# Performance work log

Measured on AMD Instinct MI355X. Metric: run time of the kernel, lower is better.

Reference implementation:

```python
import jax, jax.numpy as jnp
import numpy as np

IMG = 448; P = 16; C = 3; D = 512; DC = 8; DS = 4
NH = IMG // P            # 28 patches per side
NPATCH = NH * NH         # 784
PDIM = C * P * P         # 768
BATCH = 32
EPS = 1e-5


def setup_inputs() -> dict:
    key = jax.random.key(0)
    ks = jax.random.split(key, 10)
    def lin(k, fan_in, shape):
        bound = 1.0 / np.sqrt(fan_in)
        return jax.random.uniform(k, shape, jnp.float32, -bound, bound)
    return {
        "images": jax.random.normal(ks[0], (BATCH, C, IMG, IMG), jnp.float32),
        "W_patch": lin(ks[1], PDIM, (PDIM, D)),
        "b_patch": jnp.zeros((D,), jnp.float32),
        "pos_embed": jax.random.normal(ks[2], (1, NPATCH, D), jnp.float32) * 0.02,
        "W_coord": lin(ks[3], D, (D, DC)),
        "b_coord": jnp.zeros((DC,), jnp.float32),
        "W_spinor": lin(ks[4], D, (D, DS)),
        "b_spinor": jnp.zeros((DS,), jnp.float32),
        "W_embed": lin(ks[5], DC, (DC, D)),
        "b_embed": jnp.zeros((D,), jnp.float32),
        "ln_gamma": jnp.ones((D,), jnp.float32),
        "ln_beta": jnp.zeros((D,), jnp.float32),
        "W_out": lin(ks[6], D, (D, D)),
        "b_out": jnp.zeros((D,), jnp.float32),
    }


def reference(images, W_patch, b_patch, pos_embed, W_coord, b_coord,
              W_spinor, b_spinor, W_embed, b_embed,
              ln_gamma, ln_beta, W_out, b_out):
    B = images.shape[0]
    # patchify == F.unfold(kernel=stride=P).transpose(1,2):
    # patches[b, bh*NH+bw, c*P*P + i*P + j] = images[b, c, bh*P+i, bw*P+j]
    patches = images.reshape(B, C, NH, P, NH, P)
    patches = patches.transpose(0, 2, 4, 1, 3, 5).reshape(B, NPATCH, PDIM)
    # patch embed + positional embedding  -> (B, NPATCH, D)
    x = patches @ W_patch + b_patch + pos_embed
    # manifold projection: coords (B,N,DC), spinor (B,N,DS)
    coords = x @ W_coord + b_coord
    spinor = x @ W_spinor + b_spinor
    # K0 scalar bilinear: psi^T psi -> (B, N)
    K0 = jnp.sum(spinor * spinor, axis=-1)
    # embed back from manifold coords -> (B, N, D)
    x_manifold = coords @ W_embed + b_embed
    # K0-modulated remix + residual
    x_enh = x_manifold * K0[..., None] + x
    # output projection: LayerNorm -> Linear
    mu = jnp.mean(x_enh, axis=-1, keepdims=True)
    var = jnp.mean(jnp.square(x_enh - mu), axis=-1, keepdims=True)
    x_norm = (x_enh - mu) * jax.lax.rsqrt(var + EPS) * ln_gamma + ln_beta
    return x_norm @ W_out + b_out
```

## Files before the change

### kernel.cpp

```cpp
#include <hip/hip_runtime.h>
#include <hip/hip_bf16.h>
#include <stdint.h>


typedef __bf16 bf16_t;
typedef bf16_t bf16x8 __attribute__((ext_vector_type(8)));
typedef bf16_t bf16x4 __attribute__((ext_vector_type(4)));
typedef float  f32x4  __attribute__((ext_vector_type(4)));

#define IMG     448
#define PSZ     16
#define NHP     28
#define NPATCH  784
#define PDIM    768
#define DMODEL  512
#define MROWS   25088

__device__ __forceinline__ void gload16(void* lds, const void* g) {
  __builtin_amdgcn_global_load_lds(
      (__attribute__((address_space(1))) void*)(uintptr_t)g,
      (__attribute__((address_space(3))) void*)lds,
      16, 0, 0);
}

__global__ __launch_bounds__(256) void prep_all(
    const float* __restrict__ Wp, const float* __restrict__ Wo,
    const float* __restrict__ Wc, const float* __restrict__ Ws,
    bf16_t* __restrict__ WpT, bf16_t* __restrict__ WoT,
    bf16_t* __restrict__ Wcsg)
{
  __shared__ float t[64][65];
  const int tid = threadIdx.x;
  const int blk = blockIdx.x;

  if (blk >= 160) {
    for (int idx = tid; idx < 8192; idx += 256) {
      const int r = idx >> 9, n = idx & 511;
      float v = 0.f;
      if (r < 8)       v = Wc[n * 8 + r];
      else if (r < 12) v = Ws[n * 4 + (r - 8)];
      Wcsg[idx] = (bf16_t)v;
    }
    return;
  }

  const float* src;  bf16_t* dst;  int K, N, bx, by;
  if (blk < 96) { src = Wp; dst = WpT; K = PDIM;   N = DMODEL;
                  bx = (blk & 7) * 64;        by = (blk >> 3) * 64; }
  else          { src = Wo; dst = WoT; K = DMODEL; N = DMODEL;
                  bx = ((blk - 96) & 7) * 64; by = ((blk - 96) >> 3) * 64; }

  const int tx = tid & 63, ty = tid >> 6;
  #pragma unroll
  for (int r = ty; r < 64; r += 4)
    t[r][tx] = src[(size_t)(by + r) * N + (bx + tx)];
  __syncthreads();
  #pragma unroll
  for (int r = ty; r < 64; r += 4)
    dst[(size_t)(bx + r) * K + (by + tx)] = (bf16_t)t[tx][r];
}

__global__ __launch_bounds__(256) void patchify_bf16(
    const float* __restrict__ images, bf16_t* __restrict__ Apat)
{
  __shared__ bf16_t t[16][456];
  const int tid = threadIdx.x;
  const int bid = blockIdx.x;
  const int b = bid / 84, rem = bid % 84;
  const int c = rem / 28, ph = rem % 28;
  const float* src = images + ((size_t)(b * 3 + c) * IMG + ph * PSZ) * IMG;

  #pragma unroll
  for (int idx = tid; idx < 16 * 112; idx += 256) {
    const int i = idx / 112, x4 = idx % 112;
    const float4 v = *(const float4*)(src + (size_t)i * IMG + x4 * 4);
    bf16x4 w;
    w[0] = (bf16_t)v.x; w[1] = (bf16_t)v.y; w[2] = (bf16_t)v.z; w[3] = (bf16_t)v.w;
    *(bf16x4*)&t[i][x4 * 4] = w;
  }
  __syncthreads();

  const size_t mbase = (size_t)b * NPATCH + (size_t)ph * NHP;
  #pragma unroll
  for (int idx = tid; idx < 28 * 64; idx += 256) {
    const int pw = idx >> 6, e = idx & 63;
    const int i = e >> 2, j4 = e & 3;
    const bf16x4 w = *(const bf16x4*)&t[i][pw * 16 + j4 * 4];
    *(bf16x4*)&Apat[(mbase + pw) * PDIM + c * 256 + i * 16 + j4 * 4] = w;
  }
}

template<int KDIM, int EPI>
__global__ __launch_bounds__(256) void gemm_bf16(
    const bf16_t* __restrict__ A, const bf16_t* __restrict__ BT,
    const float* __restrict__ bias, const float* __restrict__ pos,
    void* __restrict__ outp)
{
  __shared__ bf16_t As[64 * 64];
  __shared__ bf16_t Bs[128 * 64];
  constexpr int NT = KDIM / 64;

  const int tid  = threadIdx.x;
  const int orig = blockIdx.x;
  const int wg   = (orig & 7) * 196 + (orig >> 3);
  const int n0   = (wg & 3) * 128;
  const int m0   = (wg >> 2) * 64;

  const int wave = tid >> 6, lane = tid & 63;

  const int ra = lane >> 3;
  const int ca = (lane & 7) ^ ra;
  const bf16_t* ag = A  + (size_t)(m0 + wave * 8 + ra) * KDIM + ca * 8;
  const bf16_t* bg = BT + (size_t)(n0 + wave * 8 + ra) * KDIM + ca * 8;
  bf16_t* al0 = As + (wave * 8) * 64;
  bf16_t* al1 = As + (wave * 8 + 32) * 64;
  bf16_t* bl0 = Bs + (wave * 8) * 64;
  bf16_t* bl1 = Bs + (wave * 8 + 32) * 64;
  bf16_t* bl2 = Bs + (wave * 8 + 64) * 64;
  bf16_t* bl3 = Bs + (wave * 8 + 96) * 64;

  const int wm = (wave >> 1) * 32;
  const int wn = (wave & 1) * 64;
  const int lr = lane & 15;
  const int lt = lane >> 4;

  f32x4 acc[2][4] = {};

  for (int t = 0; t < NT; ++t) {
    const int k0 = t * 64;
    __syncthreads();
    gload16(al0, ag + k0);
    gload16(al1, ag + 32 * KDIM + k0);
    gload16(bl0, bg + k0);
    gload16(bl1, bg + 32 * KDIM + k0);
    gload16(bl2, bg + 64 * KDIM + k0);
    gload16(bl3, bg + 96 * KDIM + k0);
    __syncthreads();

    #pragma unroll
    for (int ks = 0; ks < 2; ++ks) {
      const int c = ks * 4 + lt;
      bf16x8 af[2], bfr[4];
      #pragma unroll
      for (int i = 0; i < 2; ++i) {
        const int row = wm + i * 16 + lr;
        af[i] = *(const bf16x8*)&As[row * 64 + ((c ^ (row & 7)) * 8)];
      }
      #pragma unroll
      for (int j = 0; j < 4; ++j) {
        const int row = wn + j * 16 + lr;
        bfr[j] = *(const bf16x8*)&Bs[row * 64 + ((c ^ (row & 7)) * 8)];
      }
      #pragma unroll
      for (int i = 0; i < 2; ++i)
        #pragma unroll
        for (int j = 0; j < 4; ++j)
          acc[i][j] = __builtin_amdgcn_mfma_f32_16x16x32_bf16(af[i], bfr[j], acc[i][j], 0, 0, 0);
    }
  }

  const int q4 = lt << 2;
  const int colb = n0 + wn;
  #pragma unroll
  for (int i = 0; i < 2; ++i) {
    #pragma unroll
    for (int r = 0; r < 4; ++r) {
      const int mm = m0 + wm + i * 16 + q4 + r;
      if (EPI == 0) {
        const int pp = mm % NPATCH;
        const float* pe = pos + (size_t)pp * DMODEL;
        bf16_t* orow = (bf16_t*)outp + (size_t)mm * DMODEL;
        #pragma unroll
        for (int j = 0; j < 4; ++j) {
          const int nn = colb + j * 16 + lr;
          orow[nn] = (bf16_t)(acc[i][j][r] + bias[nn] + pe[nn]);
        }
      } else {
        float* orow = (float*)outp + (size_t)mm * DMODEL;
        #pragma unroll
        for (int j = 0; j < 4; ++j) {
          const int nn = colb + j * 16 + lr;
          orow[nn] = acc[i][j][r] + bias[nn];
        }
      }
    }
  }
}

__global__ __launch_bounds__(256) void manifold_v6(
    bf16_t* __restrict__ x, const bf16_t* __restrict__ Wcsg,
    const float* __restrict__ b_coord, const float* __restrict__ b_spinor,
    const float* __restrict__ We, const float* __restrict__ be,
    const float* __restrict__ gamma, const float* __restrict__ beta)
{
  __shared__ float pbuf[2][2][16][12];

  const int tid  = threadIdx.x;
  const int w    = tid >> 6;
  const int lane = tid & 63;
  const int rg   = w & 1;
  const int kh   = w >> 1;
  const int lr   = lane & 15;
  const int lk   = (lane >> 4) << 3;
  const int q4   = (lane >> 4) << 2;
  const size_t mbase = (size_t)blockIdx.x * 32;

  const bf16_t* xrow = x + (mbase + rg * 16 + lr) * DMODEL + kh * 256 + lk;
  const bf16_t* wrow = Wcsg + lr * DMODEL + kh * 256 + lk;
  f32x4 acc1 = {0.f, 0.f, 0.f, 0.f};
  #pragma unroll
  for (int ks = 0; ks < 8; ++ks) {
    const bf16x8 bf = *(const bf16x8*)(xrow + ks * 32);
    const bf16x8 wf = *(const bf16x8*)(wrow + ks * 32);
    acc1 = __builtin_amdgcn_mfma_f32_16x16x32_bf16(wf, bf, acc1, 0, 0, 0);
  }
  if (q4 < 12) {
    #pragma unroll
    for (int r = 0; r < 4; ++r) pbuf[kh][rg][lr][q4 + r] = acc1[r];
  }
  __syncthreads();

  const int n0 = lane * 8;
  f32x4 wlo[8], whi[8];
  #pragma unroll
  for (int dc = 0; dc < 8; ++dc) {
    wlo[dc] = *(const f32x4*)&We[dc * DMODEL + n0];
    whi[dc] = *(const f32x4*)&We[dc * DMODEL + n0 + 4];
  }
  const f32x4 beL = *(const f32x4*)&be[n0];
  const f32x4 beH = *(const f32x4*)&be[n0 + 4];
  const f32x4 gL  = *(const f32x4*)&gamma[n0];
  const f32x4 gH  = *(const f32x4*)&gamma[n0 + 4];
  const f32x4 btL = *(const f32x4*)&beta[n0];
  const f32x4 btH = *(const f32x4*)&beta[n0 + 4];
  float bc[8], bs[4];
  #pragma unroll
  for (int dc = 0; dc < 8; ++dc) bc[dc] = b_coord[dc];
  #pragma unroll
  for (int ds = 0; ds < 4; ++ds) bs[ds] = b_spinor[ds];

  #pragma unroll 2
  for (int rr = 0; rr < 8; ++rr) {
    const int rloc = w * 8 + rr;
    const int rg2  = rloc >> 4, r16 = rloc & 15;
    const float* p0 = &pbuf[0][rg2][r16][0];
    const float* p1 = &pbuf[1][rg2][r16][0];
    float c[8];
    #pragma unroll
    for (int dc = 0; dc < 8; ++dc) c[dc] = p0[dc] + p1[dc] + bc[dc];
    float k0 = 0.f;
    #pragma unroll
    for (int ds = 0; ds < 4; ++ds) {
      const float s = p0[8 + ds] + p1[8 + ds] + bs[ds];
      k0 += s * s;
    }

    const size_t row = mbase + rloc;
    const bf16x8 xv = *(const bf16x8*)(x + row * DMODEL + n0);

    float v[8];
    float s1 = 0.f, s2 = 0.f;
    #pragma unroll
    for (int e = 0; e < 4; ++e) {
      float xm = beL[e];
      #pragma unroll
      for (int dc = 0; dc < 8; ++dc) xm += c[dc] * wlo[dc][e];
      const float vv = xm * k0 + (float)xv[e];
      v[e] = vv; s1 += vv; s2 += vv * vv;
    }
    #pragma unroll
    for (int e = 0; e < 4; ++e) {
      float xm = beH[e];
      #pragma unroll
      for (int dc = 0; dc < 8; ++dc) xm += c[dc] * whi[dc][e];
      const float vv = xm * k0 + (float)xv[4 + e];
      v[4 + e] = vv; s1 += vv; s2 += vv * vv;
    }

    #pragma unroll
    for (int off = 1; off <= 32; off <<= 1) {
      s1 += __shfl_xor(s1, off, 64);
      s2 += __shfl_xor(s2, off, 64);
    }
    const float mu  = s1 * (1.f / 512.f);
    const float var = s2 * (1.f / 512.f) - mu * mu;
    const float rs  = rsqrtf(var + 1e-5f);

    bf16x8 o;
    #pragma unroll
    for (int e = 0; e < 4; ++e) {
      o[e]     = (bf16_t)((v[e]     - mu) * rs * gL[e] + btL[e]);
      o[4 + e] = (bf16_t)((v[4 + e] - mu) * rs * gH[e] + btH[e]);
    }
    *(bf16x8*)(x + row * DMODEL + n0) = o;
  }
}

extern "C" void kernel_launch(void* const* d_in, const int* in_sizes, int n_in,
                              void* d_out, int out_size, void* d_ws, size_t ws_size,
                              hipStream_t stream)
{
  const float* images    = (const float*)d_in[0];
  const float* W_patch   = (const float*)d_in[1];
  const float* b_patch   = (const float*)d_in[2];
  const float* pos_embed = (const float*)d_in[3];
  const float* W_coord   = (const float*)d_in[4];
  const float* b_coord   = (const float*)d_in[5];
  const float* W_spinor  = (const float*)d_in[6];
  const float* b_spinor  = (const float*)d_in[7];
  const float* W_embed   = (const float*)d_in[8];
  const float* b_embed   = (const float*)d_in[9];
  const float* ln_gamma  = (const float*)d_in[10];
  const float* ln_beta   = (const float*)d_in[11];
  const float* W_out     = (const float*)d_in[12];
  const float* b_out     = (const float*)d_in[13];
  float* out = (float*)d_out;

  const size_t SZ_APAT = (size_t)MROWS * PDIM * 2;
  const size_t SZ_X    = (size_t)MROWS * DMODEL * 2;
  const size_t SZ_WPT  = (size_t)DMODEL * PDIM * 2;
  const size_t SZ_WOT  = (size_t)DMODEL * DMODEL * 2;

  char* ws = (char*)d_ws;
  char* p  = ws;
  bf16_t* Apat = (bf16_t*)p;   p += SZ_APAT;
  bf16_t* x    = (bf16_t*)p;   p += SZ_X;
  bf16_t* WpT  = (bf16_t*)p;   p += SZ_WPT;
  bf16_t* WoT  = (bf16_t*)p;   p += SZ_WOT;
  bf16_t* Wcsg = (bf16_t*)p;

  hipLaunchKernelGGL(prep_all, dim3(161), dim3(256), 0, stream,
                     W_patch, W_out, W_coord, W_spinor, WpT, WoT, Wcsg);

  hipLaunchKernelGGL(patchify_bf16, dim3(32 * 3 * 28), dim3(256), 0, stream,
                     images, Apat);
  hipLaunchKernelGGL((gemm_bf16<PDIM, 0>), dim3(1568), dim3(256), 0, stream,
                     Apat, WpT, b_patch, pos_embed, (void*)x);

  hipLaunchKernelGGL(manifold_v6, dim3(MROWS / 32), dim3(256), 0, stream,
                     x, Wcsg, b_coord, b_spinor, W_embed, b_embed, ln_gamma, ln_beta);

  hipLaunchKernelGGL((gemm_bf16<DMODEL, 1>), dim3(1568), dim3(256), 0, stream,
                     x, WoT, b_out, (const float*)nullptr, (void*)out);
}
```

Before: 108.2 us.

## Double-buffer GEMM K-loop with 32-wide tiles and fuse weight prep into patchify

The bf16 GEMM now uses two 32-wide K stages in LDS with a new swizzle. The next stage is prefetched via direct-to-LDS loads while the MFMAs run on the current one, replacing the two-barrier load-then-compute loop. The weight transpose/prep kernel and the patchify kernel are merged into one launch with block-range dispatch, saving a launch and letting both run concurrently. Halving the K tile doubles the iteration and barrier count, and the single vmcnt(0) wait per step may limit how much overlap is gained.

```diff
diff --git a/kernel.cpp b/kernel.cpp
--- a/kernel.cpp
+++ b/kernel.cpp
@@ -23,17 +23,18 @@
       16, 0, 0);
 }
 
-__global__ __launch_bounds__(256) void prep_all(
+__global__ __launch_bounds__(256) void prep_patchify(
     const float* __restrict__ Wp, const float* __restrict__ Wo,
     const float* __restrict__ Wc, const float* __restrict__ Ws,
+    const float* __restrict__ images,
     bf16_t* __restrict__ WpT, bf16_t* __restrict__ WoT,
-    bf16_t* __restrict__ Wcsg)
+    bf16_t* __restrict__ Wcsg, bf16_t* __restrict__ Apat)
 {
-  __shared__ float t[64][65];
+  __shared__ __align__(16) char shmem[64 * 65 * 4];
   const int tid = threadIdx.x;
   const int blk = blockIdx.x;
 
-  if (blk >= 160) {
+  if (blk == 160) {
     for (int idx = tid; idx < 8192; idx += 256) {
       const int r = idx >> 9, n = idx & 511;
       float v = 0.f;
@@ -44,28 +45,26 @@
     return;
   }
 
-  const float* src;  bf16_t* dst;  int K, N, bx, by;
-  if (blk < 96) { src = Wp; dst = WpT; K = PDIM;   N = DMODEL;
-                  bx = (blk & 7) * 64;        by = (blk >> 3) * 64; }
-  else          { src = Wo; dst = WoT; K = DMODEL; N = DMODEL;
-                  bx = ((blk - 96) & 7) * 64; by = ((blk - 96) >> 3) * 64; }
-
-  const int tx = tid & 63, ty = tid >> 6;
-  #pragma unroll
-  for (int r = ty; r < 64; r += 4)
-    t[r][tx] = src[(size_t)(by + r) * N + (bx + tx)];
-  __syncthreads();
-  #pragma unroll
-  for (int r = ty; r < 64; r += 4)
-    dst[(size_t)(bx + r) * K + (by + tx)] = (bf16_t)t[tx][r];
-}
-
-__global__ __launch_bounds__(256) void patchify_bf16(
-    const float* __restrict__ images, bf16_t* __restrict__ Apat)
-{
-  __shared__ bf16_t t[16][456];
-  const int tid = threadIdx.x;
-  const int bid = blockIdx.x;
+  if (blk < 160) {
+    float (*t)[65] = (float(*)[65])shmem;
+    const float* src;  bf16_t* dst;  int K, N, bx, by;
+    if (blk < 96) { src = Wp; dst = WpT; K = PDIM;   N = DMODEL;
+                    bx = (blk & 7) * 64;        by = (blk >> 3) * 64; }
+    else          { src = Wo; dst = WoT; K = DMODEL; N = DMODEL;
+                    bx = ((blk - 96) & 7) * 64; by = ((blk - 96) >> 3) * 64; }
+    const int tx = tid & 63, ty = tid >> 6;
+    #pragma unroll
+    for (int r = ty; r < 64; r += 4)
+      t[r][tx] = src[(size_t)(by + r) * N + (bx + tx)];
+    __syncthreads();
+    #pragma unroll
+    for (int r = ty; r < 64; r += 4)
+      dst[(size_t)(bx + r) * K + (by + tx)] = (bf16_t)t[tx][r];
+    return;
+  }
+
+  bf16_t (*t)[456] = (bf16_t(*)[456])shmem;
+  const int bid = blk - 161;
   const int b = bid / 84, rem = bid % 84;
   const int c = rem / 28, ph = rem % 28;
   const float* src = images + ((size_t)(b * 3 + c) * IMG + ph * PSZ) * IMG;
@@ -96,9 +95,9 @@
     const float* __restrict__ bias, const float* __restrict__ pos,
     void* __restrict__ outp)
 {
-  __shared__ bf16_t As[64 * 64];
-  __shared__ bf16_t Bs[128 * 64];
-  constexpr int NT = KDIM / 64;
+  __shared__ bf16_t As[2][64 * 32];
+  __shared__ bf16_t Bs[2][128 * 32];
+  constexpr int NT = KDIM / 32;
 
   const int tid  = threadIdx.x;
   const int orig = blockIdx.x;
@@ -108,54 +107,59 @@
 
   const int wave = tid >> 6, lane = tid & 63;
 
-  const int ra = lane >> 3;
-  const int ca = (lane & 7) ^ ra;
-  const bf16_t* ag = A  + (size_t)(m0 + wave * 8 + ra) * KDIM + ca * 8;
-  const bf16_t* bg = BT + (size_t)(n0 + wave * 8 + ra) * KDIM + ca * 8;
-  bf16_t* al0 = As + (wave * 8) * 64;
-  bf16_t* al1 = As + (wave * 8 + 32) * 64;
-  bf16_t* bl0 = Bs + (wave * 8) * 64;
-  bf16_t* bl1 = Bs + (wave * 8 + 32) * 64;
-  bf16_t* bl2 = Bs + (wave * 8 + 64) * 64;
-  bf16_t* bl3 = Bs + (wave * 8 + 96) * 64;
+  const int row16 = lane >> 2;
+  const int ch    = lane & 3;
+  const int swz   = (row16 & 3) ^ ((row16 >> 2) & 3);
+  const int ca4   = ch ^ swz;
+
+  const bf16_t* ag  = A  + (size_t)(m0 + wave * 16 + row16)      * KDIM + ca4 * 8;
+  const bf16_t* bg0 = BT + (size_t)(n0 + wave * 32 + row16)      * KDIM + ca4 * 8;
+  const bf16_t* bg1 = BT + (size_t)(n0 + wave * 32 + 16 + row16) * KDIM + ca4 * 8;
 
   const int wm = (wave >> 1) * 32;
   const int wn = (wave & 1) * 64;
   const int lr = lane & 15;
   const int lt = lane >> 4;
 
+  auto STAGE = [&](int buf, int k0) {
+    gload16(&As[buf][(wave * 16) * 32],      ag  + k0);
+    gload16(&Bs[buf][(wave * 32) * 32],      bg0 + k0);
+    gload16(&Bs[buf][(wave * 32 + 16) * 32], bg1 + k0);
+  };
+
   f32x4 acc[2][4] = {};
 
+  STAGE(0, 0);
+  asm volatile("s_waitcnt vmcnt(0)" ::: "memory");
+  __builtin_amdgcn_s_barrier();
+
+  int buf = 0;
   for (int t = 0; t < NT; ++t) {
-    const int k0 = t * 64;
-    __syncthreads();
-    gload16(al0, ag + k0);
-    gload16(al1, ag + 32 * KDIM + k0);
-    gload16(bl0, bg + k0);
-    gload16(bl1, bg + 32 * KDIM + k0);
-    gload16(bl2, bg + 64 * KDIM + k0);
-    gload16(bl3, bg + 96 * KDIM + k0);
-    __syncthreads();
-
-    #pragma unroll
-    for (int ks = 0; ks < 2; ++ks) {
-      const int c = ks * 4 + lt;
-      bf16x8 af[2], bfr[4];
+    if (t + 1 < NT) STAGE(buf ^ 1, (t + 1) * 32);
+
+    bf16x8 af[2], bfr[4];
+    #pragma unroll
+    for (int i = 0; i < 2; ++i) {
+      const int r = wm + i * 16 + lr;
+      const int slot = lt ^ (r & 3) ^ ((r >> 2) & 3);
+      af[i] = *(const bf16x8*)&As[buf][r * 32 + slot * 8];
+    }
+    #pragma unroll
+    for (int j = 0; j < 4; ++j) {
+      const int r = wn + j * 16 + lr;
+      const int slot = lt ^ (r & 3) ^ ((r >> 2) & 3);
+      bfr[j] = *(const bf16x8*)&Bs[buf][r * 32 + slot * 8];
+    }
+    #pragma unroll
+    for (int i = 0; i < 2; ++i)
       #pragma unroll
-      for (int i = 0; i < 2; ++i) {
-        const int row = wm + i * 16 + lr;
-        af[i] = *(const bf16x8*)&As[row * 64 + ((c ^ (row & 7)) * 8)];
-      }
-      #pragma unroll
-      for (int j = 0; j < 4; ++j) {
-        const int row = wn + j * 16 + lr;
-        bfr[j] = *(const bf16x8*)&Bs[row * 64 + ((c ^ (row & 7)) * 8)];
-      }
-      #pragma unroll
-      for (int i = 0; i < 2; ++i)
-        #pragma unroll
-        for (int j = 0; j < 4; ++j)
-          acc[i][j] = __builtin_amdgcn_mfma_f32_16x16x32_bf16(af[i], bfr[j], acc[i][j], 0, 0, 0);
+      for (int j = 0; j < 4; ++j)
+        acc[i][j] = __builtin_amdgcn_mfma_f32_16x16x32_bf16(af[i], bfr[j], acc[i][j], 0, 0, 0);
+
+    if (t + 1 < NT) {
+      asm volatile("s_waitcnt vmcnt(0)" ::: "memory");
+      __builtin_amdgcn_s_barrier();
+      buf ^= 1;
     }
   }
 
@@ -329,11 +333,10 @@
   bf16_t* WoT  = (bf16_t*)p;   p += SZ_WOT;
   bf16_t* Wcsg = (bf16_t*)p;
 
-  hipLaunchKernelGGL(prep_all, dim3(161), dim3(256), 0, stream,
-                     W_patch, W_out, W_coord, W_spinor, WpT, WoT, Wcsg);
-
-  hipLaunchKernelGGL(patchify_bf16, dim3(32 * 3 * 28), dim3(256), 0, stream,
-                     images, Apat);
+  hipLaunchKernelGGL(prep_patchify, dim3(161 + 32 * 3 * 28), dim3(256), 0, stream,
+                     W_patch, W_out, W_coord, W_spinor, images,
+                     WpT, WoT, Wcsg, Apat);
+
   hipLaunchKernelGGL((gemm_bf16<PDIM, 0>), dim3(1568), dim3(256), 0, stream,
                      Apat, WpT, b_patch, pos_embed, (void*)x);
 
```

After: 117.1 us. 1.08x slower.
